# Kernel tuning notes

Measured on AMD Instinct MI355X. Metric: run time of the kernel, lower is better.

The kernel has to match this reference:

```python
import jax, jax.numpy as jnp
import numpy as np

LX = LY = KS = 14            # lengthX, lengthY, kernel_size
IN_BOND = 4
HID = 4                      # hidden_bond
CH = 2                       # channel
OUT = 10                     # output_dim
N = 32768                    # batch
LENGTH = LX * LY             # 196 sequential contraction steps
P = (LX - KS + 1) * (LY - KS + 1)  # number of patches (=1 here)
STD = 0.01
EPS = 1e-5                   # BatchNorm1d default eps


def setup_inputs() -> dict:
    key = jax.random.key(0)
    k0, k1, k2, k3 = jax.random.split(key, 4)
    x = jax.random.normal(k0, (N, IN_BOND, LX, LY), jnp.float32)
    # weights1[0]: [in_bond, hidden, channel]
    w_first = STD * jax.random.normal(k1, (IN_BOND, HID, CH), jnp.float32)
    # weights1[1..length-2]: [hidden, in_bond, hidden, channel], stacked
    w_mid = STD * jax.random.normal(k2, (LENGTH - 2, HID, IN_BOND, HID, CH), jnp.float32)
    # weights1[length-1]: [hidden, in_bond, output_dim, channel]
    w_last = STD * jax.random.normal(k3, (HID, IN_BOND, OUT, CH), jnp.float32)
    # shared BatchNorm1d(hidden) affine params
    gamma = jnp.ones((HID,), jnp.float32)
    beta = jnp.zeros((HID,), jnp.float32)
    return {"x": x, "w_first": w_first, "w_mid": w_mid, "w_last": w_last,
            "gamma": gamma, "beta": beta}


def reference(x, w_first, w_mid, w_last, gamma, beta):
    n = x.shape[0]
    # Patch extraction -> InputBucket [N, in_bond, KS*KS, P]
    buckets = []
    for k in range(LX - KS + 1):          # static, size 1 with defaults
        for l in range(LY - KS + 1):
            buckets.append(x[:, :, k:k + KS, l:l + KS].reshape(n, IN_BOND, KS * KS))
    ib = jnp.stack(buckets, axis=3)       # [N, in_bond, KS*KS, P]

    # Step 0: tensordot over in_bond, then permute -> y 'nbcr' = [N, P, CH, HID]
    y = jnp.einsum('nip,ihc->npch', ib[:, :, 0, :], w_first)

    # Middle steps 1..LENGTH-2 as a scan (strict sequential dependency chain)
    mids = jnp.moveaxis(ib[:, :, 1:LENGTH - 1, :], 2, 0)  # [LENGTH-2, N, in_bond, P]

    def step(y, inp):
        xi, w = inp  # xi: [N, in_bond, P]; w: [HID(r), IN_BOND(i), HID(h), CH(c)]
        # contra_w_d after permute: [N, P, CH, HID_left(r), HID_right(h)]
        contra = jnp.einsum('nip,rihc->npcrh', xi, w)
        y_new = jnp.einsum('npcr,npcrh->ncph', y, contra)  # 'ncbl': [N, CH, P, HID]
        # BatchNorm1d(HID) in training mode over flattened batch (biased var)
        flat = y_new.reshape(-1, HID)
        mean = jnp.mean(flat, axis=0)
        var = jnp.var(flat, axis=0)
        yb = (flat - mean) * jax.lax.rsqrt(var + EPS) * gamma + beta
        # faithful to torch's .view(-1, P, CH, HID) memory reinterpretation
        return yb.reshape(n, P, CH, HID), None

    y, _ = jax.lax.scan(step, y, (mids, w_mid))

    # Last step: -> [N, P, CH, HID, OUT] then einsum 'nbcr,nbcrl->nbcl'
    contra = jnp.einsum('nip,rioc->npcro', ib[:, :, LENGTH - 1, :], w_last)
    out = jnp.einsum('npcr,npcro->npco', y, contra)  # [N, P, CH, OUT]
    return out
```

## Files before the change

### kernel.cpp

```cpp
#include <hip/hip_runtime.h>

#define NSAMP 32768
#define INB   4
#define HIDN  4
#define CHN   2
#define OUTD  10
#define NPIX  196
#define NMID  194
#define BLK   256
#define SPT   2
#define NBLK  (NSAMP / (BLK * SPT))
#define INV_ROWS 1.52587890625e-05f
#define BN_EPS 1e-5f
#define LINEF 32
#define WS_FLOATS ((size_t)NMID * 9 * LINEF)

__device__ __forceinline__ float xcomp(const float4& v, int j) {
    return j == 0 ? v.x : j == 1 ? v.y : j == 2 ? v.z : v.w;
}

__device__ __forceinline__ void mid_step(
    int t, const float xv[SPT][INB], float y[SPT][CHN][HIDN],
    const float* __restrict__ wm,
    const float gm[HIDN], const float bt[HIDN],
    float* __restrict__ ws, float (*pb)[8], int tid, unsigned int nblk)
{
    const float* w = wm + (long)t * (HIDN * INB * HIDN * CHN);
    float yn[SPT][CHN][HIDN];
#pragma unroll
    for (int s = 0; s < SPT; ++s)
#pragma unroll
        for (int c = 0; c < CHN; ++c)
#pragma unroll
            for (int h = 0; h < HIDN; ++h) yn[s][c][h] = 0.f;

#pragma unroll
    for (int s = 0; s < SPT; ++s)
#pragma unroll
        for (int r = 0; r < HIDN; ++r)
#pragma unroll
            for (int i = 0; i < INB; ++i) {
                float p0 = y[s][0][r] * xv[s][i];
                float p1 = y[s][1][r] * xv[s][i];
                const float* wri = w + r * (INB * HIDN * CHN) + i * (HIDN * CHN);
#pragma unroll
                for (int h = 0; h < HIDN; ++h) {
                    yn[s][0][h] = fmaf(p0, wri[h * CHN + 0], yn[s][0][h]);
                    yn[s][1][h] = fmaf(p1, wri[h * CHN + 1], yn[s][1][h]);
                }
            }
    float red[8];
#pragma unroll
    for (int h = 0; h < HIDN; ++h) {
        float sm = 0.f, sq = 0.f;
#pragma unroll
        for (int s = 0; s < SPT; ++s) {
            sm += yn[s][0][h] + yn[s][1][h];
            sq += yn[s][0][h] * yn[s][0][h] + yn[s][1][h] * yn[s][1][h];
        }
        red[h] = sm; red[4 + h] = sq;
    }
#pragma unroll
    for (int j = 0; j < 8; ++j)
#pragma unroll
        for (int off = 32; off > 0; off >>= 1)
            red[j] += __shfl_down(red[j], off);
    int wv = tid >> 6;
    if ((tid & 63) == 0) {
#pragma unroll
        for (int j = 0; j < 8; ++j) pb[wv][j] = red[j];
    }
    __syncthreads();
    float* slb = ws + (size_t)t * 9 * LINEF;
    unsigned int* cnt = (unsigned int*)(slb + 8 * LINEF);
    if (tid < 8) {
        float s = pb[0][tid] + pb[1][tid] + pb[2][tid] + pb[3][tid];
        atomicAdd(&slb[tid * LINEF], s);
    }
    if (tid == 0) {
        asm volatile("s_waitcnt vmcnt(0)" ::: "memory");
        __hip_atomic_fetch_add(cnt, 1u, __ATOMIC_RELAXED, __HIP_MEMORY_SCOPE_AGENT);
        while (__hip_atomic_load(cnt, __ATOMIC_RELAXED, __HIP_MEMORY_SCOPE_AGENT) < nblk)
            __builtin_amdgcn_s_sleep(1);
    }
    __syncthreads();
    float sm[8];
#pragma unroll
    for (int j = 0; j < 8; ++j)
        sm[j] = __hip_atomic_load(&slb[j * LINEF], __ATOMIC_RELAXED,
                                  __HIP_MEMORY_SCOPE_AGENT);
#pragma unroll
    for (int h = 0; h < HIDN; ++h) {
        float m  = sm[h] * INV_ROWS;
        float v  = fmaf(-m, m, sm[4 + h] * INV_ROWS);
        float is = rsqrtf(v + BN_EPS) * gm[h];
        float sh = bt[h] - m * is;
#pragma unroll
        for (int s = 0; s < SPT; ++s) {
            y[s][0][h] = fmaf(yn[s][0][h], is, sh);
            y[s][1][h] = fmaf(yn[s][1][h], is, sh);
        }
    }
}

__global__ __launch_bounds__(BLK, 1)
void ttbn_main(const float* __restrict__ x,  const float* __restrict__ wf,
               const float* __restrict__ wm, const float* __restrict__ wl,
               const float* __restrict__ gamma, const float* __restrict__ beta,
               float* __restrict__ out, float* __restrict__ ws)
{
    __shared__ float pb[BLK / 64][8];
    const int tid = threadIdx.x;
    const unsigned int nblk = gridDim.x;

    float gm[HIDN], bt[HIDN];
#pragma unroll
    for (int h = 0; h < HIDN; ++h) { gm[h] = gamma[h]; bt[h] = beta[h]; }

    const float* xn[SPT];
    long nidx[SPT];
#pragma unroll
    for (int s = 0; s < SPT; ++s) {
        nidx[s] = (long)blockIdx.x * (BLK * SPT) + s * BLK + tid;
        xn[s]   = x + nidx[s] * (INB * NPIX);
    }

    float4 xg[SPT][INB];
    float  y[SPT][CHN][HIDN];

#pragma unroll
    for (int s = 0; s < SPT; ++s)
#pragma unroll
        for (int i = 0; i < INB; ++i)
            xg[s][i] = *reinterpret_cast<const float4*>(xn[s] + i * NPIX);

#pragma unroll
    for (int s = 0; s < SPT; ++s)
#pragma unroll
        for (int c = 0; c < CHN; ++c)
#pragma unroll
            for (int h = 0; h < HIDN; ++h) {
                float acc = 0.f;
#pragma unroll
                for (int i = 0; i < INB; ++i)
                    acc = fmaf(xg[s][i].x, wf[i * (HIDN * CHN) + h * CHN + c], acc);
                y[s][c][h] = acc;
            }
#pragma unroll
    for (int slp = 1; slp < 4; ++slp) {
        float xv[SPT][INB];
#pragma unroll
        for (int s = 0; s < SPT; ++s)
#pragma unroll
            for (int i = 0; i < INB; ++i) xv[s][i] = xcomp(xg[s][i], slp);
        mid_step(slp - 1, xv, y, wm, gm, bt, ws, pb, tid, nblk);
    }

#pragma unroll 1
    for (int g = 1; g < 48; ++g) {
#pragma unroll
        for (int s = 0; s < SPT; ++s)
#pragma unroll
            for (int i = 0; i < INB; ++i)
                xg[s][i] = *reinterpret_cast<const float4*>(xn[s] + i * NPIX + g * 4);
#pragma unroll
        for (int slp = 0; slp < 4; ++slp) {
            float xv[SPT][INB];
#pragma unroll
            for (int s = 0; s < SPT; ++s)
#pragma unroll
                for (int i = 0; i < INB; ++i) xv[s][i] = xcomp(xg[s][i], slp);
            mid_step(g * 4 + slp - 1, xv, y, wm, gm, bt, ws, pb, tid, nblk);
        }
    }

#pragma unroll
    for (int s = 0; s < SPT; ++s)
#pragma unroll
        for (int i = 0; i < INB; ++i)
            xg[s][i] = *reinterpret_cast<const float4*>(xn[s] + i * NPIX + 192);
#pragma unroll
    for (int slp = 0; slp < 3; ++slp) {
        float xv[SPT][INB];
#pragma unroll
        for (int s = 0; s < SPT; ++s)
#pragma unroll
            for (int i = 0; i < INB; ++i) xv[s][i] = xcomp(xg[s][i], slp);
        mid_step(191 + slp, xv, y, wm, gm, bt, ws, pb, tid, nblk);
    }
#pragma unroll
    for (int s = 0; s < SPT; ++s) {
        float xv[INB];
#pragma unroll
        for (int i = 0; i < INB; ++i) xv[i] = xg[s][i].w;
        float o0[OUTD], o1[OUTD];
#pragma unroll
        for (int od = 0; od < OUTD; ++od) { o0[od] = 0.f; o1[od] = 0.f; }
#pragma unroll
        for (int r = 0; r < HIDN; ++r)
#pragma unroll
            for (int i = 0; i < INB; ++i) {
                float p0 = y[s][0][r] * xv[i];
                float p1 = y[s][1][r] * xv[i];
                const float* wri = wl + r * (INB * OUTD * CHN) + i * (OUTD * CHN);
#pragma unroll
                for (int od = 0; od < OUTD; ++od) {
                    o0[od] = fmaf(p0, wri[od * CHN + 0], o0[od]);
                    o1[od] = fmaf(p1, wri[od * CHN + 1], o1[od]);
                }
            }
        float tmp[20];
#pragma unroll
        for (int od = 0; od < OUTD; ++od) { tmp[od] = o0[od]; tmp[10 + od] = o1[od]; }
        float4* o4 = reinterpret_cast<float4*>(out + nidx[s] * (CHN * OUTD));
#pragma unroll
        for (int q = 0; q < 5; ++q)
            o4[q] = make_float4(tmp[q * 4], tmp[q * 4 + 1], tmp[q * 4 + 2], tmp[q * 4 + 3]);
    }
}

extern "C" void kernel_launch(void* const* d_in, const int* in_sizes, int n_in,
                              void* d_out, int out_size, void* d_ws, size_t ws_size,
                              hipStream_t stream) {
    const float* x     = (const float*)d_in[0];
    const float* wf    = (const float*)d_in[1];
    const float* wm    = (const float*)d_in[2];
    const float* wl    = (const float*)d_in[3];
    const float* gamma = (const float*)d_in[4];
    const float* beta  = (const float*)d_in[5];
    float*       out   = (float*)d_out;
    float*       ws    = (float*)d_ws;

    hipMemsetAsync(d_ws, 0, WS_FLOATS * sizeof(float), stream);

    void* args[] = { &x, &wf, &wm, &wl, &gamma, &beta, &out, &ws };
    hipLaunchCooperativeKernel((void*)ttbn_main, dim3(NBLK), dim3(BLK),
                               args, 0, stream);
}
```

Measured before the change: 982.9 us.

## Replace atomic-counter grid barrier with per-block sentinel slots and wave-polled reduction

Each block now publishes its partial BatchNorm sums as packed 64-bit values into its own slot per step. Every block then polls all 64 blocks' slots in parallel, one lane per block, until no sentinel remains, and reduces them with wave shuffles. This removes the float atomicAdds, the counter increment and the single-thread spin-then-syncthreads barrier from the critical path of 194 sequential steps. The costs are more polling traffic (64 lanes each reading four slots per block), a larger workspace memset, and a reliance on the 64-bit stores being seen atomically. The reduction order is also fixed, so results are deterministic.

```diff
diff --git a/kernel.cpp b/kernel.cpp
--- a/kernel.cpp
+++ b/kernel.cpp
@@ -12,8 +12,8 @@
 #define NBLK  (NSAMP / (BLK * SPT))
 #define INV_ROWS 1.52587890625e-05f
 #define BN_EPS 1e-5f
-#define LINEF 32
-#define WS_FLOATS ((size_t)NMID * 9 * LINEF)
+#define SENT  0xFFFFFFFFFFFFFFFFull
+#define WS_BYTES ((size_t)NMID * NBLK * 4 * sizeof(unsigned long long))
 
 __device__ __forceinline__ float xcomp(const float4& v, int j) {
     return j == 0 ? v.x : j == 1 ? v.y : j == 2 ? v.z : v.w;
@@ -23,7 +23,7 @@
     int t, const float xv[SPT][INB], float y[SPT][CHN][HIDN],
     const float* __restrict__ wm,
     const float gm[HIDN], const float bt[HIDN],
-    float* __restrict__ ws, float (*pb)[8], int tid, unsigned int nblk)
+    unsigned long long* __restrict__ slots, float (*pb)[8], int tid)
 {
     const float* w = wm + (long)t * (HIDN * INB * HIDN * CHN);
     float yn[SPT][CHN][HIDN];
@@ -65,30 +65,38 @@
 #pragma unroll
         for (int off = 32; off > 0; off >>= 1)
             red[j] += __shfl_down(red[j], off);
-    int wv = tid >> 6;
-    if ((tid & 63) == 0) {
+    const int wv = tid >> 6, ln = tid & 63;
+    if (ln == 0) {
 #pragma unroll
         for (int j = 0; j < 8; ++j) pb[wv][j] = red[j];
     }
     __syncthreads();
-    float* slb = ws + (size_t)t * 9 * LINEF;
-    unsigned int* cnt = (unsigned int*)(slb + 8 * LINEF);
-    if (tid < 8) {
-        float s = pb[0][tid] + pb[1][tid] + pb[2][tid] + pb[3][tid];
-        atomicAdd(&slb[tid * LINEF], s);
-    }
-    if (tid == 0) {
-        asm volatile("s_waitcnt vmcnt(0)" ::: "memory");
-        __hip_atomic_fetch_add(cnt, 1u, __ATOMIC_RELAXED, __HIP_MEMORY_SCOPE_AGENT);
-        while (__hip_atomic_load(cnt, __ATOMIC_RELAXED, __HIP_MEMORY_SCOPE_AGENT) < nblk)
-            __builtin_amdgcn_s_sleep(1);
-    }
-    __syncthreads();
+    if (tid < 4) {
+        float lo = pb[0][2 * tid]     + pb[1][2 * tid]     + pb[2][2 * tid]     + pb[3][2 * tid];
+        float hi = pb[0][2 * tid + 1] + pb[1][2 * tid + 1] + pb[2][2 * tid + 1] + pb[3][2 * tid + 1];
+        unsigned long long v = ((unsigned long long)__float_as_uint(hi) << 32)
+                             |  (unsigned long long)__float_as_uint(lo);
+        __hip_atomic_store(&slots[((size_t)t * NBLK + blockIdx.x) * 4 + tid], v,
+                           __ATOMIC_RELAXED, __HIP_MEMORY_SCOPE_AGENT);
+    }
+    const unsigned long long* ps = &slots[((size_t)t * NBLK + ln) * 4];
+    unsigned long long q0, q1, q2, q3;
+    do {
+        q0 = __hip_atomic_load(&ps[0], __ATOMIC_RELAXED, __HIP_MEMORY_SCOPE_AGENT);
+        q1 = __hip_atomic_load(&ps[1], __ATOMIC_RELAXED, __HIP_MEMORY_SCOPE_AGENT);
+        q2 = __hip_atomic_load(&ps[2], __ATOMIC_RELAXED, __HIP_MEMORY_SCOPE_AGENT);
+        q3 = __hip_atomic_load(&ps[3], __ATOMIC_RELAXED, __HIP_MEMORY_SCOPE_AGENT);
+    } while (!__all(q0 != SENT && q1 != SENT && q2 != SENT && q3 != SENT));
     float sm[8];
+    sm[0] = __uint_as_float((unsigned)q0); sm[1] = __uint_as_float((unsigned)(q0 >> 32));
+    sm[2] = __uint_as_float((unsigned)q1); sm[3] = __uint_as_float((unsigned)(q1 >> 32));
+    sm[4] = __uint_as_float((unsigned)q2); sm[5] = __uint_as_float((unsigned)(q2 >> 32));
+    sm[6] = __uint_as_float((unsigned)q3); sm[7] = __uint_as_float((unsigned)(q3 >> 32));
 #pragma unroll
     for (int j = 0; j < 8; ++j)
-        sm[j] = __hip_atomic_load(&slb[j * LINEF], __ATOMIC_RELAXED,
-                                  __HIP_MEMORY_SCOPE_AGENT);
+#pragma unroll
+        for (int off = 1; off < 64; off <<= 1)
+            sm[j] += __shfl_xor(sm[j], off);
 #pragma unroll
     for (int h = 0; h < HIDN; ++h) {
         float m  = sm[h] * INV_ROWS;
@@ -107,11 +115,10 @@
 void ttbn_main(const float* __restrict__ x,  const float* __restrict__ wf,
                const float* __restrict__ wm, const float* __restrict__ wl,
                const float* __restrict__ gamma, const float* __restrict__ beta,
-               float* __restrict__ out, float* __restrict__ ws)
+               float* __restrict__ out, unsigned long long* __restrict__ slots)
 {
     __shared__ float pb[BLK / 64][8];
     const int tid = threadIdx.x;
-    const unsigned int nblk = gridDim.x;
 
     float gm[HIDN], bt[HIDN];
 #pragma unroll
@@ -153,7 +160,7 @@
         for (int s = 0; s < SPT; ++s)
 #pragma unroll
             for (int i = 0; i < INB; ++i) xv[s][i] = xcomp(xg[s][i], slp);
-        mid_step(slp - 1, xv, y, wm, gm, bt, ws, pb, tid, nblk);
+        mid_step(slp - 1, xv, y, wm, gm, bt, slots, pb, tid);
     }
 
 #pragma unroll 1
@@ -170,7 +177,7 @@
             for (int s = 0; s < SPT; ++s)
 #pragma unroll
                 for (int i = 0; i < INB; ++i) xv[s][i] = xcomp(xg[s][i], slp);
-            mid_step(g * 4 + slp - 1, xv, y, wm, gm, bt, ws, pb, tid, nblk);
+            mid_step(g * 4 + slp - 1, xv, y, wm, gm, bt, slots, pb, tid);
         }
     }
 
@@ -186,7 +193,7 @@
         for (int s = 0; s < SPT; ++s)
 #pragma unroll
             for (int i = 0; i < INB; ++i) xv[s][i] = xcomp(xg[s][i], slp);
-        mid_step(191 + slp, xv, y, wm, gm, bt, ws, pb, tid, nblk);
+        mid_step(191 + slp, xv, y, wm, gm, bt, slots, pb, tid);
     }
 #pragma unroll
     for (int s = 0; s < SPT; ++s) {
@@ -229,11 +236,11 @@
     const float* gamma = (const float*)d_in[4];
     const float* beta  = (const float*)d_in[5];
     float*       out   = (float*)d_out;
-    float*       ws    = (float*)d_ws;
-
-    hipMemsetAsync(d_ws, 0, WS_FLOATS * sizeof(float), stream);
-
-    void* args[] = { &x, &wf, &wm, &wl, &gamma, &beta, &out, &ws };
+    unsigned long long* slots = (unsigned long long*)d_ws;
+
+    hipMemsetAsync(d_ws, 0xFF, WS_BYTES, stream);
+
+    void* args[] = { &x, &wf, &wm, &wl, &gamma, &beta, &out, &slots };
     hipLaunchCooperativeKernel((void*)ttbn_main, dim3(NBLK), dim3(BLK),
                                args, 0, stream);
 }
```

After: 936.8 us. 1.05x faster.
